# Kernel optimization log

Measured on AMD Instinct MI355X. Metric: run time of the kernel, lower is better.

The kernel has to match this reference:

```python
import jax, jax.numpy as jnp
import numpy as np

EMB = 1024
HEADS = 16
HEAD_SIZE = EMB // HEADS


def setup_inputs() -> dict:
    key = jax.random.key(0)
    ks = jax.random.split(key, 10)
    s = 1.0 / np.sqrt(EMB)
    return {
        "x": jax.random.normal(ks[0], (2, 2048, EMB), dtype=jnp.float32),
        "ln_gamma": jnp.ones((EMB,), jnp.float32),
        "ln_beta": jnp.zeros((EMB,), jnp.float32),
        "Wq": jax.random.normal(ks[1], (EMB, EMB), jnp.float32) * s,
        "bq": jnp.zeros((EMB,), jnp.float32),
        "Wk": jax.random.normal(ks[2], (EMB, EMB), jnp.float32) * s,
        "bk": jnp.zeros((EMB,), jnp.float32),
        "Wv": jax.random.normal(ks[3], (EMB, EMB), jnp.float32) * s,
        "bv": jnp.zeros((EMB,), jnp.float32),
        "Wo": jax.random.normal(ks[4], (EMB, EMB), jnp.float32) * s,
        "bo": jnpps if False else jnp.zeros((EMB,), jnp.float32),
    }


def _layernorm(x, gamma, beta, eps=1e-5):
    mu = jnp.mean(x, axis=-1, keepdims=True)
    var = jnp.mean(jnp.square(x - mu), axis=-1, keepdims=True)
    return (x - mu) * jax.lax.rsqrt(var + eps) * gamma + beta


def reference(x, ln_gamma, ln_beta, Wq, bq, Wk, bk, Wv, bv, Wo, bo):
    B, L, D = x.shape
    h = _layernorm(x, ln_gamma, ln_beta)
    # projections -> [B, H, L, hd]
    def split_heads(t):
        return t.reshape(B, L, HEADS, HEAD_SIZE).transpose(0, 2, 1, 3)
    q = split_heads(h @ Wq.T + bq)
    k = split_heads(h @ Wk.T + bk)
    v = split_heads(h @ Wv.T + bv)
    scale = HEAD_SIZE ** (-0.5)
    w = jnp.einsum("bhqd,bhkd->bhqk", q, k) * scale  # [B,H,L,L]
    w = jax.nn.softmax(w, axis=-1)
    o = jnp.einsum("bhqk,bhkd->bhqd", w, v)
    o = o.transpose(0, 2, 1, 3).reshape(B, L, D)
    o = o @ Wo.T + bo
    return x + o
```

## Files before the change

### kernel.cpp

```cpp
#include <hip/hip_runtime.h>
#include <math.h>

#define B_   2
#define L_   2048
#define EMB_ 1024
#define H_   16
#define HD_  64
#define M_   (B_ * L_)

typedef __bf16 bf16x8 __attribute__((ext_vector_type(8)));
typedef __bf16 bf16x4 __attribute__((ext_vector_type(4)));
typedef float floatx16 __attribute__((ext_vector_type(16)));

typedef __attribute__((address_space(1))) const void GV;
typedef __attribute__((address_space(3))) void LV;

#define MFMA32(a, b, c) __builtin_amdgcn_mfma_f32_32x32x16_bf16((a), (b), (c), 0, 0, 0)

__global__ __launch_bounds__(256) void cvt_w_kernel(
        const float* __restrict__ s0, const float* __restrict__ s1,
        const float* __restrict__ s2, const float* __restrict__ s3,
        __bf16* __restrict__ d0, __bf16* __restrict__ d1,
        __bf16* __restrict__ d2, __bf16* __restrict__ d3) {
    int z = blockIdx.y;
    const float* s = (z == 0) ? s0 : (z == 1) ? s1 : (z == 2) ? s2 : s3;
    __bf16* d = (z == 0) ? d0 : (z == 1) ? d1 : (z == 2) ? d2 : d3;
    size_t base = (size_t)(blockIdx.x * 256 + threadIdx.x) * 16;
#pragma unroll
    for (int j = 0; j < 4; ++j) {
        float4 f = *(const float4*)(s + base + j * 4);
        bf16x4 t;
        t[0] = (__bf16)f.x; t[1] = (__bf16)f.y; t[2] = (__bf16)f.z; t[3] = (__bf16)f.w;
        *(bf16x4*)(d + base + j * 4) = t;
    }
}

__global__ __launch_bounds__(256) void ln_kernel(
        const float* __restrict__ x, const float* __restrict__ gamma,
        const float* __restrict__ beta, __bf16* __restrict__ h) {
    int row = blockIdx.x;
    int tid = threadIdx.x;
    const float* xr = x + (size_t)row * EMB_;
    float4 v = *(const float4*)(xr + tid * 4);
    float s  = v.x + v.y + v.z + v.w;
    float ss = v.x * v.x + v.y * v.y + v.z * v.z + v.w * v.w;
    for (int off = 32; off; off >>= 1) {
        s  += __shfl_down(s, off, 64);
        ss += __shfl_down(ss, off, 64);
    }
    __shared__ float s1[4], s2[4];
    int wid = tid >> 6;
    if ((tid & 63) == 0) { s1[wid] = s; s2[wid] = ss; }
    __syncthreads();
    if (tid == 0) {
        float a = s1[0] + s1[1] + s1[2] + s1[3];
        float b = s2[0] + s2[1] + s2[2] + s2[3];
        float mu = a / EMB_;
        float var = b / EMB_ - mu * mu;
        s1[0] = mu;
        s2[0] = rsqrtf(var + 1e-5f);
    }
    __syncthreads();
    float mu = s1[0], rstd = s2[0];
    float4 g4 = *(const float4*)(gamma + tid * 4);
    float4 b4 = *(const float4*)(beta + tid * 4);
    bf16x4 o;
    o[0] = (__bf16)((v.x - mu) * rstd * g4.x + b4.x);
    o[1] = (__bf16)((v.y - mu) * rstd * g4.y + b4.y);
    o[2] = (__bf16)((v.z - mu) * rstd * g4.z + b4.z);
    o[3] = (__bf16)((v.w - mu) * rstd * g4.w + b4.w);
    *(bf16x4*)(h + (size_t)row * EMB_ + tid * 4) = o;
}

__device__ __forceinline__ void stage_tile128(const __bf16* gbase, __bf16* lds,
                                              int wave, int lane) {
    int srow = lane >> 3;
    int gch0 = lane & 7;
#pragma unroll
    for (int s = 0; s < 4; ++s) {
        int seg = wave * 4 + s;
        int row = seg * 8 + srow;
        int g = gch0 ^ (row & 7);
        __builtin_amdgcn_global_load_lds(
            (GV*)(gbase + (size_t)row * EMB_ + g * 8),
            (LV*)(lds + seg * 512 + lane * 8), 16, 0, 0);
    }
}

__global__ __launch_bounds__(256) void gemm_qkv_mfma(
        const __bf16* __restrict__ A,
        const __bf16* __restrict__ Wqb, const __bf16* __restrict__ Wkb,
        const __bf16* __restrict__ Wvb,
        const float* __restrict__ bq, const float* __restrict__ bk,
        const float* __restrict__ bv,
        __bf16* __restrict__ Qo, __bf16* __restrict__ Ko,
        __bf16* __restrict__ Vto) {
    __shared__ __bf16 As[128 * 64];
    __shared__ __bf16 Bs[128 * 64];
    const int z = blockIdx.z;
    const __bf16* W = (z == 0) ? Wqb : (z == 1) ? Wkb : Wvb;
    const float* bias = (z == 0) ? bq : (z == 1) ? bk : bv;

    int tid = threadIdx.x, wave = tid >> 6, lane = tid & 63;
    int wm = wave >> 1, wn = wave & 1;
    int quad = lane >> 5;
    int bm = blockIdx.y * 128, bn = blockIdx.x * 128;

    floatx16 acc[2][2];
#pragma unroll
    for (int i = 0; i < 2; ++i)
#pragma unroll
        for (int j = 0; j < 2; ++j)
#pragma unroll
            for (int r = 0; r < 16; ++r) acc[i][j][r] = 0.f;

    for (int k0 = 0; k0 < EMB_; k0 += 64) {
        __syncthreads();
        stage_tile128(A + (size_t)bm * EMB_ + k0, As, wave, lane);
        stage_tile128(W + (size_t)bn * EMB_ + k0, Bs, wave, lane);
        __syncthreads();
#pragma unroll
        for (int s = 0; s < 4; ++s) {
            int g = 2 * s + quad;
            int r0 = wm * 64 + (lane & 31);
            int r1 = r0 + 32;
            int c0 = wn * 64 + (lane & 31);
            int c1 = c0 + 32;
            bf16x8 a0 = *(const bf16x8*)&As[r0 * 64 + ((g ^ (r0 & 7)) * 8)];
            bf16x8 a1 = *(const bf16x8*)&As[r1 * 64 + ((g ^ (r1 & 7)) * 8)];
            bf16x8 b0 = *(const bf16x8*)&Bs[c0 * 64 + ((g ^ (c0 & 7)) * 8)];
            bf16x8 b1 = *(const bf16x8*)&Bs[c1 * 64 + ((g ^ (c1 & 7)) * 8)];
            acc[0][0] = MFMA32(a0, b0, acc[0][0]);
            acc[0][1] = MFMA32(a0, b1, acc[0][1]);
            acc[1][0] = MFMA32(a1, b0, acc[1][0]);
            acc[1][1] = MFMA32(a1, b1, acc[1][1]);
        }
    }

    float qscale = (z == 0) ? 0.125f : 1.0f;
#pragma unroll
    for (int mb = 0; mb < 2; ++mb) {
#pragma unroll
        for (int nb = 0; nb < 2; ++nb) {
            int col = bn + wn * 64 + nb * 32 + (lane & 31);
            float bv_ = bias[col];
            if (z < 2) {
                __bf16* dst = (z == 0) ? Qo : Ko;
#pragma unroll
                for (int r = 0; r < 16; ++r) {
                    int row = bm + wm * 64 + mb * 32 + (r & 3) + 8 * (r >> 2) + 4 * quad;
                    dst[(size_t)row * EMB_ + col] = (__bf16)((acc[mb][nb][r] + bv_) * qscale);
                }
            } else {
                int hh = col >> 6, d = col & 63;
#pragma unroll
                for (int rb = 0; rb < 4; ++rb) {
                    int row = bm + wm * 64 + mb * 32 + 8 * rb + 4 * quad;
                    int b = row >> 11, l = row & (L_ - 1);
                    bf16x4 t;
#pragma unroll
                    for (int a = 0; a < 4; ++a) t[a] = (__bf16)(acc[mb][nb][4 * rb + a] + bv_);
                    *(bf16x4*)(Vto + ((size_t)(b * H_ + hh) * HD_ + d) * L_ + l) = t;
                }
            }
        }
    }
}

__global__ __launch_bounds__(256) void gemm_out_mfma(
        const __bf16* __restrict__ A, const __bf16* __restrict__ W,
        const float* __restrict__ bias, const float* __restrict__ x,
        float* __restrict__ out) {
    __shared__ __bf16 As[128 * 64];
    __shared__ __bf16 Bs[128 * 64];
    int tid = threadIdx.x, wave = tid >> 6, lane = tid & 63;
    int wm = wave >> 1, wn = wave & 1;
    int quad = lane >> 5;
    int bm = blockIdx.y * 128, bn = blockIdx.x * 128;

    floatx16 acc[2][2];
#pragma unroll
    for (int i = 0; i < 2; ++i)
#pragma unroll
        for (int j = 0; j < 2; ++j)
#pragma unroll
            for (int r = 0; r < 16; ++r) acc[i][j][r] = 0.f;

    for (int k0 = 0; k0 < EMB_; k0 += 64) {
        __syncthreads();
        stage_tile128(A + (size_t)bm * EMB_ + k0, As, wave, lane);
        stage_tile128(W + (size_t)bn * EMB_ + k0, Bs, wave, lane);
        __syncthreads();
#pragma unroll
        for (int s = 0; s < 4; ++s) {
            int g = 2 * s + quad;
            int r0 = wm * 64 + (lane & 31);
            int r1 = r0 + 32;
            int c0 = wn * 64 + (lane & 31);
            int c1 = c0 + 32;
            bf16x8 a0 = *(const bf16x8*)&As[r0 * 64 + ((g ^ (r0 & 7)) * 8)];
            bf16x8 a1 = *(const bf16x8*)&As[r1 * 64 + ((g ^ (r1 & 7)) * 8)];
            bf16x8 b0 = *(const bf16x8*)&Bs[c0 * 64 + ((g ^ (c0 & 7)) * 8)];
            bf16x8 b1 = *(const bf16x8*)&Bs[c1 * 64 + ((g ^ (c1 & 7)) * 8)];
            acc[0][0] = MFMA32(a0, b0, acc[0][0]);
            acc[0][1] = MFMA32(a0, b1, acc[0][1]);
            acc[1][0] = MFMA32(a1, b0, acc[1][0]);
            acc[1][1] = MFMA32(a1, b1, acc[1][1]);
        }
    }

#pragma unroll
    for (int mb = 0; mb < 2; ++mb) {
#pragma unroll
        for (int nb = 0; nb < 2; ++nb) {
            int col = bn + wn * 64 + nb * 32 + (lane & 31);
            float bv_ = bias[col];
#pragma unroll
            for (int r = 0; r < 16; ++r) {
                size_t row = bm + wm * 64 + mb * 32 + (r & 3) + 8 * (r >> 2) + 4 * quad;
                out[row * EMB_ + col] = acc[mb][nb][r] + bv_ + x[row * EMB_ + col];
            }
        }
    }
}

#define PSTR 88

__global__ __launch_bounds__(256) void attn_mfma(
        const __bf16* __restrict__ Q,
        const __bf16* __restrict__ K,
        const __bf16* __restrict__ Vt,
        __bf16* __restrict__ O) {
    __shared__ __bf16 Ks[64 * 64];
    __shared__ __bf16 Vs[64 * 64];
    __shared__ __bf16 Ps[4][32 * PSTR];

    int tid = threadIdx.x, wave = tid >> 6, lane = tid & 63;
    int quad = lane >> 5;
    int bh = blockIdx.y;
    int b = bh >> 4, h = bh & 15;
    int q0 = blockIdx.x * 128 + wave * 32;
    const size_t tok0 = (size_t)b * L_;

    bf16x8 qf[4];
    {
        const __bf16* qp = Q + (tok0 + q0 + (lane & 31)) * EMB_ + h * HD_ + quad * 8;
#pragma unroll
        for (int s = 0; s < 4; ++s) qf[s] = *(const bf16x8*)(qp + s * 16);
    }

    floatx16 oacc[2];
#pragma unroll
    for (int d = 0; d < 2; ++d)
#pragma unroll
        for (int r = 0; r < 16; ++r) oacc[d][r] = 0.f;
    float lacc[16];
#pragma unroll
    for (int r = 0; r < 16; ++r) lacc[r] = 0.f;

    const __bf16* Kbase = K + tok0 * EMB_ + h * HD_;
    const __bf16* Vbase = Vt + (size_t)bh * HD_ * L_;
    __bf16* Pw = &Ps[wave][0];

    int srow = lane >> 3;
    int gch0 = lane & 7;

    for (int kt = 0; kt < L_; kt += 64) {
        __syncthreads();
#pragma unroll
        for (int s = 0; s < 2; ++s) {
            int seg = wave + s * 4;
            int row = seg * 8 + srow;
            int g = gch0 ^ (row & 7);
            __builtin_amdgcn_global_load_lds(
                (GV*)(Kbase + (size_t)(kt + row) * EMB_ + g * 8),
                (LV*)(Ks + seg * 512 + lane * 8), 16, 0, 0);
            __builtin_amdgcn_global_load_lds(
                (GV*)(Vbase + (size_t)row * L_ + kt + g * 8),
                (LV*)(Vs + seg * 512 + lane * 8), 16, 0, 0);
        }
        __syncthreads();

#pragma unroll
        for (int nb = 0; nb < 2; ++nb) {
            floatx16 sacc;
#pragma unroll
            for (int r = 0; r < 16; ++r) sacc[r] = 0.f;
#pragma unroll
            for (int s = 0; s < 4; ++s) {
                int krow = nb * 32 + (lane & 31);
                int g = 2 * s + quad;
                bf16x8 kf = *(const bf16x8*)&Ks[krow * 64 + ((g ^ (krow & 7)) * 8)];
                sacc = MFMA32(qf[s], kf, sacc);
            }
#pragma unroll
            for (int r = 0; r < 16; ++r) {
                float p = __expf(sacc[r]);
                lacc[r] += p;
                int qr = (r & 3) + 8 * (r >> 2) + 4 * quad;
                Pw[qr * PSTR + nb * 32 + (lane & 31)] = (__bf16)p;
            }
        }

#pragma unroll
        for (int s = 0; s < 4; ++s) {
            bf16x8 pf = *(const bf16x8*)&Pw[(lane & 31) * PSTR + s * 16 + quad * 8];
#pragma unroll
            for (int db = 0; db < 2; ++db) {
                int drow = db * 32 + (lane & 31);
                int g = 2 * s + quad;
                bf16x8 vf = *(const bf16x8*)&Vs[drow * 64 + ((g ^ (drow & 7)) * 8)];
                oacc[db] = MFMA32(pf, vf, oacc[db]);
            }
        }
    }

#pragma unroll
    for (int r = 0; r < 16; ++r) {
        float l = lacc[r];
        l += __shfl_xor(l, 1, 64);
        l += __shfl_xor(l, 2, 64);
        l += __shfl_xor(l, 4, 64);
        l += __shfl_xor(l, 8, 64);
        l += __shfl_xor(l, 16, 64);
        lacc[r] = 1.0f / l;
    }
#pragma unroll
    for (int db = 0; db < 2; ++db) {
        int col = h * HD_ + db * 32 + (lane & 31);
#pragma unroll
        for (int r = 0; r < 16; ++r) {
            int qr = q0 + (r & 3) + 8 * (r >> 2) + 4 * quad;
            O[(tok0 + qr) * EMB_ + col] = (__bf16)(oacc[db][r] * lacc[r]);
        }
    }
}

extern "C" void kernel_launch(void* const* d_in, const int* in_sizes, int n_in,
                              void* d_out, int out_size, void* d_ws, size_t ws_size,
                              hipStream_t stream) {
    const float* x     = (const float*)d_in[0];
    const float* gamma = (const float*)d_in[1];
    const float* beta  = (const float*)d_in[2];
    const float* Wq    = (const float*)d_in[3];
    const float* bq    = (const float*)d_in[4];
    const float* Wk    = (const float*)d_in[5];
    const float* bk    = (const float*)d_in[6];
    const float* Wv    = (const float*)d_in[7];
    const float* bv    = (const float*)d_in[8];
    const float* Wo    = (const float*)d_in[9];
    const float* bo    = (const float*)d_in[10];
    float* out = (float*)d_out;

    const size_t SLAB = (size_t)M_ * EMB_;
    const size_t WSLAB = (size_t)EMB_ * EMB_;
    char* ws = (char*)d_ws;
    __bf16* hb   = (__bf16*)ws;                       ws += SLAB * 2;
    __bf16* Qb   = (__bf16*)ws;                       ws += SLAB * 2;
    __bf16* Kb   = (__bf16*)ws;                       ws += SLAB * 2;
    __bf16* Vtb  = (__bf16*)ws;                       ws += SLAB * 2;
    __bf16* Ob   = (__bf16*)ws;                       ws += SLAB * 2;
    __bf16* Wqb  = (__bf16*)ws;                       ws += WSLAB * 2;
    __bf16* Wkb  = (__bf16*)ws;                       ws += WSLAB * 2;
    __bf16* Wvb  = (__bf16*)ws;                       ws += WSLAB * 2;
    __bf16* Wob  = (__bf16*)ws;                       ws += WSLAB * 2;

    cvt_w_kernel<<<dim3(256, 4), 256, 0, stream>>>(Wq, Wk, Wv, Wo, Wqb, Wkb, Wvb, Wob);
    ln_kernel<<<M_, 256, 0, stream>>>(x, gamma, beta, hb);
    gemm_qkv_mfma<<<dim3(EMB_ / 128, M_ / 128, 3), 256, 0, stream>>>(
        hb, Wqb, Wkb, Wvb, bq, bk, bv, Qb, Kb, Vtb);
    attn_mfma<<<dim3(L_ / 128, B_ * H_), 256, 0, stream>>>(Qb, Kb, Vtb, Ob);
    gemm_out_mfma<<<dim3(EMB_ / 128, M_ / 128), 256, 0, stream>>>(Ob, Wob, bo, x, out);
}
```

Before: 230.0 us.

## Split attention over key halves and add combine kernel; transpose MFMA layout

Splits the key loop of the attention kernel into two halves on a third grid dimension, which doubles the number of blocks from 512 to 1024. Each half writes an unnormalized bf16 partial output and a row sum, and a new combine kernel adds the two partials and normalizes. It also swaps the MFMA operand order so each lane holds one query row, which simplifies the row-sum reduction and allows XOR-swizzled bf16x4 stores of P without padding. The costs are an extra kernel launch, extra global traffic for the partials, and bf16 rounding of the partial outputs before they are combined.

Measured after the change: 223.9 us. 2.7% less time.

```diff
diff --git a/kernel.cpp b/kernel.cpp
--- a/kernel.cpp
+++ b/kernel.cpp
@@ -224,27 +224,27 @@
     }
 }
 
-#define PSTR 88
-
 __global__ __launch_bounds__(256) void attn_mfma(
         const __bf16* __restrict__ Q,
         const __bf16* __restrict__ K,
         const __bf16* __restrict__ Vt,
-        __bf16* __restrict__ O) {
+        __bf16* __restrict__ Op,
+        float* __restrict__ Lp) {
     __shared__ __bf16 Ks[64 * 64];
     __shared__ __bf16 Vs[64 * 64];
-    __shared__ __bf16 Ps[4][32 * PSTR];
+    __shared__ __bf16 Ps[4][32 * 64];
 
     int tid = threadIdx.x, wave = tid >> 6, lane = tid & 63;
-    int quad = lane >> 5;
+    int quad = lane >> 5, lq = lane & 31;
     int bh = blockIdx.y;
     int b = bh >> 4, h = bh & 15;
+    int ks = blockIdx.z;
     int q0 = blockIdx.x * 128 + wave * 32;
     const size_t tok0 = (size_t)b * L_;
 
     bf16x8 qf[4];
     {
-        const __bf16* qp = Q + (tok0 + q0 + (lane & 31)) * EMB_ + h * HD_ + quad * 8;
+        const __bf16* qp = Q + (tok0 + q0 + lq) * EMB_ + h * HD_ + quad * 8;
 #pragma unroll
         for (int s = 0; s < 4; ++s) qf[s] = *(const bf16x8*)(qp + s * 16);
     }
@@ -254,18 +254,16 @@
     for (int d = 0; d < 2; ++d)
 #pragma unroll
         for (int r = 0; r < 16; ++r) oacc[d][r] = 0.f;
-    float lacc[16];
-#pragma unroll
-    for (int r = 0; r < 16; ++r) lacc[r] = 0.f;
+    float lacc = 0.f;
 
     const __bf16* Kbase = K + tok0 * EMB_ + h * HD_;
     const __bf16* Vbase = Vt + (size_t)bh * HD_ * L_;
     __bf16* Pw = &Ps[wave][0];
-
     int srow = lane >> 3;
     int gch0 = lane & 7;
-
-    for (int kt = 0; kt < L_; kt += 64) {
+    int pq = lq & 7;
+
+    for (int kt = ks * 1024; kt < ks * 1024 + 1024; kt += 64) {
         __syncthreads();
 #pragma unroll
         for (int s = 0; s < 2; ++s) {
@@ -288,52 +286,88 @@
             for (int r = 0; r < 16; ++r) sacc[r] = 0.f;
 #pragma unroll
             for (int s = 0; s < 4; ++s) {
-                int krow = nb * 32 + (lane & 31);
+                int krow = nb * 32 + lq;
                 int g = 2 * s + quad;
                 bf16x8 kf = *(const bf16x8*)&Ks[krow * 64 + ((g ^ (krow & 7)) * 8)];
-                sacc = MFMA32(qf[s], kf, sacc);
+                sacc = MFMA32(kf, qf[s], sacc);
             }
 #pragma unroll
-            for (int r = 0; r < 16; ++r) {
-                float p = __expf(sacc[r]);
-                lacc[r] += p;
-                int qr = (r & 3) + 8 * (r >> 2) + 4 * quad;
-                Pw[qr * PSTR + nb * 32 + (lane & 31)] = (__bf16)p;
+            for (int g4 = 0; g4 < 4; ++g4) {
+                float p0 = __expf(sacc[4 * g4 + 0]);
+                float p1 = __expf(sacc[4 * g4 + 1]);
+                float p2 = __expf(sacc[4 * g4 + 2]);
+                float p3 = __expf(sacc[4 * g4 + 3]);
+                lacc += (p0 + p1) + (p2 + p3);
+                bf16x4 t;
+                t[0] = (__bf16)p0; t[1] = (__bf16)p1; t[2] = (__bf16)p2; t[3] = (__bf16)p3;
+                int c = 4 * nb + g4;
+                *(bf16x4*)&Pw[lq * 64 + ((c ^ pq) * 8) + quad * 4] = t;
             }
         }
 
 #pragma unroll
         for (int s = 0; s < 4; ++s) {
-            bf16x8 pf = *(const bf16x8*)&Pw[(lane & 31) * PSTR + s * 16 + quad * 8];
+            int c = 2 * s + quad;
+            bf16x8 pf = *(const bf16x8*)&Pw[lq * 64 + ((c ^ pq) * 8)];
 #pragma unroll
             for (int db = 0; db < 2; ++db) {
-                int drow = db * 32 + (lane & 31);
+                int drow = db * 32 + lq;
                 int g = 2 * s + quad;
                 bf16x8 vf = *(const bf16x8*)&Vs[drow * 64 + ((g ^ (drow & 7)) * 8)];
-                oacc[db] = MFMA32(pf, vf, oacc[db]);
+                oacc[db] = MFMA32(vf, pf, oacc[db]);
             }
         }
     }
 
-#pragma unroll
-    for (int r = 0; r < 16; ++r) {
-        float l = lacc[r];
-        l += __shfl_xor(l, 1, 64);
-        l += __shfl_xor(l, 2, 64);
-        l += __shfl_xor(l, 4, 64);
-        l += __shfl_xor(l, 8, 64);
-        l += __shfl_xor(l, 16, 64);
-        lacc[r] = 1.0f / l;
-    }
+    lacc += __shfl_xor(lacc, 32, 64);
+    if (lane < 32) {
+        Lp[((size_t)ks * 32 + bh) * L_ + q0 + lane] = lacc;
+    }
+
 #pragma unroll
     for (int db = 0; db < 2; ++db) {
-        int col = h * HD_ + db * 32 + (lane & 31);
-#pragma unroll
-        for (int r = 0; r < 16; ++r) {
-            int qr = q0 + (r & 3) + 8 * (r >> 2) + 4 * quad;
-            O[(tok0 + qr) * EMB_ + col] = (__bf16)(oacc[db][r] * lacc[r]);
-        }
-    }
+#pragma unroll
+        for (int g4 = 0; g4 < 4; ++g4) {
+            bf16x4 t;
+            t[0] = (__bf16)oacc[db][4 * g4 + 0];
+            t[1] = (__bf16)oacc[db][4 * g4 + 1];
+            t[2] = (__bf16)oacc[db][4 * g4 + 2];
+            t[3] = (__bf16)oacc[db][4 * g4 + 3];
+            int c = g4 + 4 * db;
+            *(bf16x4*)&Pw[lq * 64 + ((c ^ pq) * 8) + quad * 4] = t;
+        }
+    }
+    {
+        int q = lane >> 1, half = lane & 1;
+        __bf16* orow = Op + ((size_t)ks * M_ + tok0 + q0 + q) * EMB_ + h * HD_ + half * 32;
+#pragma unroll
+        for (int i = 0; i < 4; ++i) {
+            int cc = 4 * half + i;
+            bf16x8 t = *(const bf16x8*)&Pw[q * 64 + ((cc ^ (q & 7)) * 8)];
+            *(bf16x8*)(orow + i * 8) = t;
+        }
+    }
+}
+
+__global__ __launch_bounds__(256) void combine_kernel(
+        const __bf16* __restrict__ Op, const float* __restrict__ Lp,
+        __bf16* __restrict__ Ob) {
+    size_t idx = (size_t)blockIdx.x * 256 + threadIdx.x;
+    size_t t = idx >> 7;
+    int c8 = (int)(idx & 127) * 8;
+    int h = c8 >> 6;
+    int b = (int)(t >> 11);
+    int lqi = (int)(t & (L_ - 1));
+    int bh = b * H_ + h;
+    float l0 = Lp[(size_t)bh * L_ + lqi];
+    float l1 = Lp[(size_t)(32 + bh) * L_ + lqi];
+    float rl = 1.0f / (l0 + l1);
+    bf16x8 a = *(const bf16x8*)(Op + t * EMB_ + c8);
+    bf16x8 c = *(const bf16x8*)(Op + (size_t)M_ * EMB_ + t * EMB_ + c8);
+    bf16x8 o;
+#pragma unroll
+    for (int j = 0; j < 8; ++j) o[j] = (__bf16)(((float)a[j] + (float)c[j]) * rl);
+    *(bf16x8*)(Ob + t * EMB_ + c8) = o;
 }
 
 extern "C" void kernel_launch(void* const* d_in, const int* in_sizes, int n_in,
@@ -364,11 +398,14 @@
     __bf16* Wkb  = (__bf16*)ws;                       ws += WSLAB * 2;
     __bf16* Wvb  = (__bf16*)ws;                       ws += WSLAB * 2;
     __bf16* Wob  = (__bf16*)ws;                       ws += WSLAB * 2;
+    __bf16* Op   = (__bf16*)ws;                       ws += 2 * SLAB * 2;
+    float*  Lp   = (float*)ws;                        ws += 2 * 32 * (size_t)L_ * 4;
 
     cvt_w_kernel<<<dim3(256, 4), 256, 0, stream>>>(Wq, Wk, Wv, Wo, Wqb, Wkb, Wvb, Wob);
     ln_kernel<<<M_, 256, 0, stream>>>(x, gamma, beta, hb);
     gemm_qkv_mfma<<<dim3(EMB_ / 128, M_ / 128, 3), 256, 0, stream>>>(
         hb, Wqb, Wkb, Wvb, bq, bk, bv, Qb, Kb, Vtb);
-    attn_mfma<<<dim3(L_ / 128, B_ * H_), 256, 0, stream>>>(Qb, Kb, Vtb, Ob);
+    attn_mfma<<<dim3(L_ / 128, B_ * H_, 2), 256, 0, stream>>>(Qb, Kb, Vtb, Op, Lp);
+    combine_kernel<<<(M_ * EMB_ / 8) / 256, 256, 0, stream>>>(Op, Lp, Ob);
     gemm_out_mfma<<<dim3(EMB_ / 128, M_ / 128), 256, 0, stream>>>(Ob, Wob, bo, x, out);
 }
```
